# Kernel tuning notes

Measured on AMD Instinct MI355X. Metric: run time of the kernel, lower is better.

## Reference

```python
import jax, jax.numpy as jnp
import numpy as np

N, K, D = 65536, 4096, 64


def setup_inputs() -> dict:
    key = jax.random.key(0)
    kx, ke = jax.random.split(key)
    x = jax.random.normal(kx, (N, D), dtype=jnp.float32)
    embed = jax.random.normal(ke, (1, K, D), dtype=jnp.float32)
    return {"x": x, "embed": embed}


def reference(x, embed):
    # Faithful to EuclideanCodebook.forward quantization path:
    #   dist = cdist(flatten, embed, p=2)**2 ; argmin ; one_hot @ embed
    xf = x.astype(jnp.float32)            # [N, D]
    e = embed[0]                          # [K, D]
    # squared euclidean distance via expansion (== cdist(...).pow(2))
    x_sq = jnp.sum(xf * xf, axis=-1, keepdims=True)        # [N, 1]
    e_sq = jnp.sum(e * e, axis=-1)                          # [K]
    dist = jnp.maximum(x_sq + e_sq[None, :] - 2.0 * (xf @ e.T), 0.0)  # [N, K]
    embed_ind = jnp.argmin(dist, axis=-1)                   # [N]
    # one_hot @ embed is exactly a row gather of the codebook
    quantize = e[embed_ind]                                 # [N, D]
    return quantize, embed_ind[None, :]                     # embed_ind kept as [1, N] like torch
```

## Files before the change

### kernel.cpp

```cpp
#include <hip/hip_runtime.h>
#include <math.h>

#define N_ROWS 65536
#define K_CODES 4096
#define NTILES_TOTAL (K_CODES / 32)
#define K_CHUNKS 2
#define NTILES (NTILES_TOTAL / K_CHUNKS)
#define DIM 64
#define NBUF 4
#define ACC_MARGIN 0.005f

typedef __attribute__((ext_vector_type(8))) short bf16x8;
typedef __attribute__((ext_vector_type(4))) float f32x4;

__device__ inline unsigned short f2bf_rne(float f) {
    unsigned u = __float_as_uint(f);
    return (unsigned short)((u + 0x7FFFu + ((u >> 16) & 1u)) >> 16);
}
__device__ inline float bf2f(unsigned short s) {
    return __uint_as_float(((unsigned)s) << 16);
}

__global__ __launch_bounds__(256) void pack_e(const float* __restrict__ embed,
                                              short* __restrict__ e_pk,
                                              float* __restrict__ esq,
                                              float* __restrict__ esqn,
                                              int* __restrict__ count) {
    __shared__ float lds_f[2048];
    const int tile = blockIdx.x;
    const int t = threadIdx.x;
    if (tile == 0 && t == 0) *count = 0;
    const float4* src = (const float4*)(embed + (size_t)tile * 2048);
    ((float4*)lds_f)[t] = src[t];
    ((float4*)lds_f)[t + 256] = src[t + 256];
    __syncthreads();
    const int l = t & 63;
    const int kh = (t >> 6) & 1;
    const int ch = (t >> 7) & 1;
    const int base = (ch * 16 + (l & 15)) * 64 + kh * 32 + ((l >> 4) & 3) * 8;
    bf16x8 vh, vl;
#pragma unroll
    for (int j = 0; j < 8; ++j) {
        float v = lds_f[base + j];
        unsigned short h = f2bf_rne(v);
        vh[j] = (short)h;
        vl[j] = (short)f2bf_rne(v - bf2f(h));
    }
    *(bf16x8*)(e_pk + (size_t)tile * 4096 + t * 8) = vh;
    *(bf16x8*)(e_pk + (size_t)tile * 4096 + 2048 + t * 8) = vl;
    if (t < 32) {
        float s = 0.f;
#pragma unroll
        for (int d = 0; d < 64; ++d) { float v = lds_f[t * 64 + d]; s = fmaf(v, v, s); }
        esq[tile * 32 + t] = s;
        esqn[tile * 32 + t] = -0.5f * s;
    }
}

__global__ __launch_bounds__(256, 4) void vq_main(const float* __restrict__ x,
                                                  const short* __restrict__ e_pk,
                                                  const float* __restrict__ esqn,
                                                  float* __restrict__ b1s,
                                                  float* __restrict__ b2s,
                                                  int* __restrict__ i1s) {
    __shared__ __align__(16) char lds[NBUF][8192];
    __shared__ __align__(16) float lds_q[NBUF][64];
    const int tid = threadIdx.x;
    const int wid = tid >> 6;
    const int l = tid & 63;
    const int c16 = l & 15;
    const int rgrp = (l >> 4) & 3;
    const int kc = blockIdx.x & (K_CHUNKS - 1);
    const int rg = blockIdx.x >> 1;
    const int rowbase = rg * 128 + wid * 32;
    const int tile0 = kc * NTILES;

    bf16x8 ah[2][2], al[2][2];
#pragma unroll
    for (int rh = 0; rh < 2; ++rh) {
        const float* xr = x + (size_t)(rowbase + rh * 16 + c16) * DIM;
#pragma unroll
        for (int kh = 0; kh < 2; ++kh) {
            const float* p = xr + kh * 32 + rgrp * 8;
#pragma unroll
            for (int j = 0; j < 8; ++j) {
                float v = p[j];
                unsigned short h = f2bf_rne(v);
                ah[rh][kh][j] = (short)h;
                al[rh][kh][j] = (short)f2bf_rne(v - bf2f(h));
            }
        }
    }

    float b1[8], b2[8];
    int i1[8];
#pragma unroll
    for (int i = 0; i < 8; ++i) { b1[i] = -3.0e38f; b2[i] = -3.0e38f; i1[i] = 0; }

    auto stage = [&](int t, int b) {
        const char* gsrc = (const char*)e_pk + (size_t)(tile0 + t) * 8192 + tid * 16;
        __builtin_amdgcn_global_load_lds(
            (const __attribute__((address_space(1))) void*)gsrc,
            (__attribute__((address_space(3))) void*)(&lds[b][wid * 1024]), 16, 0, 0);
        __builtin_amdgcn_global_load_lds(
            (const __attribute__((address_space(1))) void*)(gsrc + 4096),
            (__attribute__((address_space(3))) void*)(&lds[b][4096 + wid * 1024]), 16, 0, 0);
        const float* qsrc = esqn + (size_t)(tile0 + t) * 32 + l;
        __builtin_amdgcn_global_load_lds(
            (const __attribute__((address_space(1))) void*)qsrc,
            (__attribute__((address_space(3))) void*)(&lds_q[b][0]), 4, 0, 0);
    };

    stage(0, 0);
    stage(1, 1);

    for (int t = 0; t < NTILES; ++t) {
        const int cur = t & (NBUF - 1);
        if (t + 2 < NTILES) stage(t + 2, (t + 2) & (NBUF - 1));
        asm volatile("s_waitcnt vmcnt(6)" ::: "memory");
        __builtin_amdgcn_sched_barrier(0);
        __builtin_amdgcn_s_barrier();
        __builtin_amdgcn_sched_barrier(0);

        const float eq0 = lds_q[cur][c16];
        const float eq1 = lds_q[cur][16 + c16];
        const int ci0 = (tile0 + t) * 32 + c16;
        const int ci1 = ci0 + 16;

        f32x4 a00 = {eq0, eq0, eq0, eq0};
        f32x4 a01 = {eq1, eq1, eq1, eq1};
        f32x4 a10 = {eq0, eq0, eq0, eq0};
        f32x4 a11 = {eq1, eq1, eq1, eq1};

        __builtin_amdgcn_s_setprio(1);
#pragma unroll
        for (int kh = 0; kh < 2; ++kh) {
            const int fo0 = ((0 * 2 + kh) * 64 + l) * 16;
            const int fo1 = ((1 * 2 + kh) * 64 + l) * 16;
            const bf16x8 bh0 = *(const bf16x8*)(&lds[cur][fo0]);
            const bf16x8 bh1 = *(const bf16x8*)(&lds[cur][fo1]);
            const bf16x8 bl0 = *(const bf16x8*)(&lds[cur][4096 + fo0]);
            const bf16x8 bl1 = *(const bf16x8*)(&lds[cur][4096 + fo1]);
            a00 = __builtin_amdgcn_mfma_f32_16x16x32_bf16(ah[0][kh], bh0, a00, 0, 0, 0);
            a01 = __builtin_amdgcn_mfma_f32_16x16x32_bf16(ah[0][kh], bh1, a01, 0, 0, 0);
            a10 = __builtin_amdgcn_mfma_f32_16x16x32_bf16(ah[1][kh], bh0, a10, 0, 0, 0);
            a11 = __builtin_amdgcn_mfma_f32_16x16x32_bf16(ah[1][kh], bh1, a11, 0, 0, 0);
            a00 = __builtin_amdgcn_mfma_f32_16x16x32_bf16(ah[0][kh], bl0, a00, 0, 0, 0);
            a01 = __builtin_amdgcn_mfma_f32_16x16x32_bf16(ah[0][kh], bl1, a01, 0, 0, 0);
            a10 = __builtin_amdgcn_mfma_f32_16x16x32_bf16(ah[1][kh], bl0, a10, 0, 0, 0);
            a11 = __builtin_amdgcn_mfma_f32_16x16x32_bf16(ah[1][kh], bl1, a11, 0, 0, 0);
            a00 = __builtin_amdgcn_mfma_f32_16x16x32_bf16(al[0][kh], bh0, a00, 0, 0, 0);
            a01 = __builtin_amdgcn_mfma_f32_16x16x32_bf16(al[0][kh], bh1, a01, 0, 0, 0);
            a10 = __builtin_amdgcn_mfma_f32_16x16x32_bf16(al[1][kh], bh0, a10, 0, 0, 0);
            a11 = __builtin_amdgcn_mfma_f32_16x16x32_bf16(al[1][kh], bh1, a11, 0, 0, 0);
        }
        __builtin_amdgcn_s_setprio(0);

#define TRACK2(V0, V1, E)                                            \
        {                                                            \
            float v0 = (V0), v1 = (V1);                              \
            bool g0 = v0 > b1[E];                                    \
            b2[E] = __builtin_amdgcn_fmed3f(v0, b1[E], b2[E]);       \
            b1[E] = fmaxf(v0, b1[E]);                                \
            i1[E] = g0 ? ci0 : i1[E];                                \
            bool g1 = v1 > b1[E];                                    \
            b2[E] = __builtin_amdgcn_fmed3f(v1, b1[E], b2[E]);       \
            b1[E] = fmaxf(v1, b1[E]);                                \
            i1[E] = g1 ? ci1 : i1[E];                                \
        }
#pragma unroll
        for (int j = 0; j < 4; ++j) {
            TRACK2(a00[j], a01[j], j)
            TRACK2(a10[j], a11[j], 4 + j)
        }
#undef TRACK2
    }

#pragma unroll
    for (int e = 0; e < 8; ++e) {
#pragma unroll
        for (int m = 1; m <= 8; m <<= 1) {
            float ob1 = __shfl_xor(b1[e], m);
            float ob2 = __shfl_xor(b2[e], m);
            int oi = __shfl_xor(i1[e], m);
            float nb2 = fmaxf(fminf(b1[e], ob1), fmaxf(b2[e], ob2));
            bool take = ob1 > b1[e];
            b1[e] = take ? ob1 : b1[e];
            i1[e] = take ? oi : i1[e];
            b2[e] = nb2;
        }
        if (c16 == 0) {
            int row = rowbase + (e >> 2) * 16 + rgrp * 4 + (e & 3);
            b1s[(size_t)kc * N_ROWS + row] = b1[e];
            b2s[(size_t)kc * N_ROWS + row] = b2[e];
            i1s[(size_t)kc * N_ROWS + row] = i1[e];
        }
    }
}

__global__ __launch_bounds__(256) void vq_merge_gather(const float* __restrict__ embed,
                                                       const float* __restrict__ b1s,
                                                       const float* __restrict__ b2s,
                                                       const int* __restrict__ i1s,
                                                       float* __restrict__ out_q,
                                                       float* __restrict__ out_ind,
                                                       int* __restrict__ list,
                                                       int* __restrict__ count) {
    int t = blockIdx.x * 256 + threadIdx.x;
    int r = t >> 3, q = t & 7;
    float ab1 = b1s[r], bb1 = b1s[N_ROWS + r];
    float ab2 = b2s[r], bb2 = b2s[N_ROWS + r];
    int ai = i1s[r], bi = i1s[N_ROWS + r];
    bool take = bb1 > ab1;
    int idx = take ? bi : ai;
    float m1 = fmaxf(ab1, bb1);
    float m2 = fmaxf(fminf(ab1, bb1), fmaxf(ab2, bb2));
    const float4* src = (const float4*)(embed + (size_t)idx * DIM + q * 8);
    float4* dst = (float4*)(out_q + (size_t)r * DIM + q * 8);
    dst[0] = src[0];
    dst[1] = src[1];
    if (q == 0) {
        out_ind[r] = (float)idx;
        if (m1 - m2 < ACC_MARGIN) {
            int p = atomicAdd(count, 1);
            list[p] = r;
        }
    }
}

__global__ __launch_bounds__(256) void vq_rescore(const float* __restrict__ x,
                                                  const float* __restrict__ embed,
                                                  const float* __restrict__ esq,
                                                  const int* __restrict__ list,
                                                  const int* __restrict__ count,
                                                  float* __restrict__ out_q,
                                                  float* __restrict__ out_ind) {
    __shared__ float xs[64];
    __shared__ float sk[256];
    __shared__ int si[256];
    const int tid = threadIdx.x;
    const int n = *count;
    for (int f = blockIdx.x; f < n; f += gridDim.x) {
        const int row = list[f];
        if (tid < 16) ((float4*)xs)[tid] = ((const float4*)(x + (size_t)row * DIM))[tid];
        __syncthreads();
        float best = 3.0e38f;
        int bi = 0;
        for (int i = 0; i < 16; ++i) {
            int c = tid + (i << 8);
            const float* e = embed + (size_t)c * DIM;
            float d0 = 0, d1 = 0, d2 = 0, d3 = 0;
#pragma unroll
            for (int d = 0; d < 64; d += 4) {
                d0 = fmaf(xs[d + 0], e[d + 0], d0);
                d1 = fmaf(xs[d + 1], e[d + 1], d1);
                d2 = fmaf(xs[d + 2], e[d + 2], d2);
                d3 = fmaf(xs[d + 3], e[d + 3], d3);
            }
            float key = fmaf(-2.f, (d0 + d1) + (d2 + d3), esq[c]);
            if (key < best) { best = key; bi = c; }
        }
        sk[tid] = best; si[tid] = bi;
        __syncthreads();
        for (int s = 128; s > 0; s >>= 1) {
            if (tid < s) {
                float ok = sk[tid + s]; int oi = si[tid + s];
                if (ok < sk[tid] || (ok == sk[tid] && oi < si[tid])) { sk[tid] = ok; si[tid] = oi; }
            }
            __syncthreads();
        }
        if (tid == 0) out_ind[row] = (float)si[0];
        if (tid < 16) {
            const float4* src = (const float4*)(embed + (size_t)si[0] * DIM);
            ((float4*)(out_q + (size_t)row * DIM))[tid] = src[tid];
        }
        __syncthreads();
    }
}

extern "C" void kernel_launch(void* const* d_in, const int* in_sizes, int n_in,
                              void* d_out, int out_size, void* d_ws, size_t ws_size,
                              hipStream_t stream) {
    const float* x = (const float*)d_in[0];
    const float* embed = (const float*)d_in[1];
    float* out = (float*)d_out;
    float* out_ind = out + (size_t)N_ROWS * DIM;

    char* ws = (char*)d_ws;
    short* e_pk = (short*)ws;
    size_t off = 1 << 20;
    float* esq = (float*)(ws + off);  off += 17 << 10;
    float* esqn = (float*)(ws + off); off += 17 << 10;
    float* b1s = (float*)(ws + off);  off += (size_t)K_CHUNKS * N_ROWS * 4;
    float* b2s = (float*)(ws + off);  off += (size_t)K_CHUNKS * N_ROWS * 4;
    int* i1s = (int*)(ws + off);      off += (size_t)K_CHUNKS * N_ROWS * 4;
    int* list = (int*)(ws + off);     off += (size_t)N_ROWS * 4;
    int* count = (int*)(ws + off);

    pack_e<<<NTILES_TOTAL, 256, 0, stream>>>(embed, e_pk, esq, esqn, count);
    vq_main<<<(N_ROWS / 128) * K_CHUNKS, 256, 0, stream>>>(x, e_pk, esqn, b1s, b2s, i1s);
    vq_merge_gather<<<N_ROWS * 8 / 256, 256, 0, stream>>>(embed, b1s, b2s, i1s,
                                                          out, out_ind, list, count);
    vq_rescore<<<512, 256, 0, stream>>>(x, embed, esq, list, count, out, out_ind);
}
```

Baseline: 146.9 us.

## Switch codebook LDS staging to double buffer with full wait and hoisted fragment loads

```diff
diff --git a/kernel.cpp b/kernel.cpp
--- a/kernel.cpp
+++ b/kernel.cpp
@@ -7,7 +7,7 @@
 #define K_CHUNKS 2
 #define NTILES (NTILES_TOTAL / K_CHUNKS)
 #define DIM 64
-#define NBUF 4
+#define NBUF 2
 #define ACC_MARGIN 0.005f
 
 typedef __attribute__((ext_vector_type(8))) short bf16x8;
@@ -112,21 +112,30 @@
     };
 
     stage(0, 0);
-    stage(1, 1);
 
     for (int t = 0; t < NTILES; ++t) {
-        const int cur = t & (NBUF - 1);
-        if (t + 2 < NTILES) stage(t + 2, (t + 2) & (NBUF - 1));
-        asm volatile("s_waitcnt vmcnt(6)" ::: "memory");
+        const int cur = t & 1;
+        asm volatile("s_waitcnt vmcnt(0) lgkmcnt(0)" ::: "memory");
         __builtin_amdgcn_sched_barrier(0);
         __builtin_amdgcn_s_barrier();
         __builtin_amdgcn_sched_barrier(0);
+        if (t + 1 < NTILES) stage(t + 1, cur ^ 1);
 
         const float eq0 = lds_q[cur][c16];
         const float eq1 = lds_q[cur][16 + c16];
         const int ci0 = (tile0 + t) * 32 + c16;
         const int ci1 = ci0 + 16;
 
+        bf16x8 bh[2][2], bl[2][2];
+#pragma unroll
+        for (int ch = 0; ch < 2; ++ch)
+#pragma unroll
+            for (int kh = 0; kh < 2; ++kh) {
+                const int fo = ((ch * 2 + kh) * 64 + l) * 16;
+                bh[ch][kh] = *(const bf16x8*)(&lds[cur][fo]);
+                bl[ch][kh] = *(const bf16x8*)(&lds[cur][4096 + fo]);
+            }
+
         f32x4 a00 = {eq0, eq0, eq0, eq0};
         f32x4 a01 = {eq1, eq1, eq1, eq1};
         f32x4 a10 = {eq0, eq0, eq0, eq0};
@@ -135,24 +144,18 @@
         __builtin_amdgcn_s_setprio(1);
 #pragma unroll
         for (int kh = 0; kh < 2; ++kh) {
-            const int fo0 = ((0 * 2 + kh) * 64 + l) * 16;
-            const int fo1 = ((1 * 2 + kh) * 64 + l) * 16;
-            const bf16x8 bh0 = *(const bf16x8*)(&lds[cur][fo0]);
-            const bf16x8 bh1 = *(const bf16x8*)(&lds[cur][fo1]);
-            const bf16x8 bl0 = *(const bf16x8*)(&lds[cur][4096 + fo0]);
-            const bf16x8 bl1 = *(const bf16x8*)(&lds[cur][4096 + fo1]);
-            a00 = __builtin_amdgcn_mfma_f32_16x16x32_bf16(ah[0][kh], bh0, a00, 0, 0, 0);
-            a01 = __builtin_amdgcn_mfma_f32_16x16x32_bf16(ah[0][kh], bh1, a01, 0, 0, 0);
-            a10 = __builtin_amdgcn_mfma_f32_16x16x32_bf16(ah[1][kh], bh0, a10, 0, 0, 0);
-            a11 = __builtin_amdgcn_mfma_f32_16x16x32_bf16(ah[1][kh], bh1, a11, 0, 0, 0);
-            a00 = __builtin_amdgcn_mfma_f32_16x16x32_bf16(ah[0][kh], bl0, a00, 0, 0, 0);
-            a01 = __builtin_amdgcn_mfma_f32_16x16x32_bf16(ah[0][kh], bl1, a01, 0, 0, 0);
-            a10 = __builtin_amdgcn_mfma_f32_16x16x32_bf16(ah[1][kh], bl0, a10, 0, 0, 0);
-            a11 = __builtin_amdgcn_mfma_f32_16x16x32_bf16(ah[1][kh], bl1, a11, 0, 0, 0);
-            a00 = __builtin_amdgcn_mfma_f32_16x16x32_bf16(al[0][kh], bh0, a00, 0, 0, 0);
-            a01 = __builtin_amdgcn_mfma_f32_16x16x32_bf16(al[0][kh], bh1, a01, 0, 0, 0);
-            a10 = __builtin_amdgcn_mfma_f32_16x16x32_bf16(al[1][kh], bh0, a10, 0, 0, 0);
-            a11 = __builtin_amdgcn_mfma_f32_16x16x32_bf16(al[1][kh], bh1, a11, 0, 0, 0);
+            a00 = __builtin_amdgcn_mfma_f32_16x16x32_bf16(ah[0][kh], bh[0][kh], a00, 0, 0, 0);
+            a01 = __builtin_amdgcn_mfma_f32_16x16x32_bf16(ah[0][kh], bh[1][kh], a01, 0, 0, 0);
+            a10 = __builtin_amdgcn_mfma_f32_16x16x32_bf16(ah[1][kh], bh[0][kh], a10, 0, 0, 0);
+            a11 = __builtin_amdgcn_mfma_f32_16x16x32_bf16(ah[1][kh], bh[1][kh], a11, 0, 0, 0);
+            a00 = __builtin_amdgcn_mfma_f32_16x16x32_bf16(ah[0][kh], bl[0][kh], a00, 0, 0, 0);
+            a01 = __builtin_amdgcn_mfma_f32_16x16x32_bf16(ah[0][kh], bl[1][kh], a01, 0, 0, 0);
+            a10 = __builtin_amdgcn_mfma_f32_16x16x32_bf16(ah[1][kh], bl[0][kh], a10, 0, 0, 0);
+            a11 = __builtin_amdgcn_mfma_f32_16x16x32_bf16(ah[1][kh], bl[1][kh], a11, 0, 0, 0);
+            a00 = __builtin_amdgcn_mfma_f32_16x16x32_bf16(al[0][kh], bh[0][kh], a00, 0, 0, 0);
+            a01 = __builtin_amdgcn_mfma_f32_16x16x32_bf16(al[0][kh], bh[1][kh], a01, 0, 0, 0);
+            a10 = __builtin_amdgcn_mfma_f32_16x16x32_bf16(al[1][kh], bh[0][kh], a10, 0, 0, 0);
+            a11 = __builtin_amdgcn_mfma_f32_16x16x32_bf16(al[1][kh], bh[1][kh], a11, 0, 0, 0);
         }
         __builtin_amdgcn_s_setprio(0);
 
```

After: 146.5 us. Within noise of the previous version (-0.2%).

## Double per-wave row tile and load codebook tiles directly to registers

Applied to the files above, without the earlier changes.

```diff
diff --git a/kernel.cpp b/kernel.cpp
--- a/kernel.cpp
+++ b/kernel.cpp
@@ -7,7 +7,6 @@
 #define K_CHUNKS 2
 #define NTILES (NTILES_TOTAL / K_CHUNKS)
 #define DIM 64
-#define NBUF 4
 #define ACC_MARGIN 0.005f
 
 typedef __attribute__((ext_vector_type(8))) short bf16x8;
@@ -57,14 +56,12 @@
     }
 }
 
-__global__ __launch_bounds__(256, 4) void vq_main(const float* __restrict__ x,
+__global__ __launch_bounds__(256, 2) void vq_main(const float* __restrict__ x,
                                                   const short* __restrict__ e_pk,
                                                   const float* __restrict__ esqn,
                                                   float* __restrict__ b1s,
                                                   float* __restrict__ b2s,
                                                   int* __restrict__ i1s) {
-    __shared__ __align__(16) char lds[NBUF][8192];
-    __shared__ __align__(16) float lds_q[NBUF][64];
     const int tid = threadIdx.x;
     const int wid = tid >> 6;
     const int l = tid & 63;
@@ -72,12 +69,12 @@
     const int rgrp = (l >> 4) & 3;
     const int kc = blockIdx.x & (K_CHUNKS - 1);
     const int rg = blockIdx.x >> 1;
-    const int rowbase = rg * 128 + wid * 32;
+    const int rowbase = rg * 256 + wid * 64;
     const int tile0 = kc * NTILES;
 
-    bf16x8 ah[2][2], al[2][2];
-#pragma unroll
-    for (int rh = 0; rh < 2; ++rh) {
+    bf16x8 ah[4][2], al[4][2];
+#pragma unroll
+    for (int rh = 0; rh < 4; ++rh) {
         const float* xr = x + (size_t)(rowbase + rh * 16 + c16) * DIM;
 #pragma unroll
         for (int kh = 0; kh < 2; ++kh) {
@@ -92,92 +89,89 @@
         }
     }
 
-    float b1[8], b2[8];
-    int i1[8];
-#pragma unroll
-    for (int i = 0; i < 8; ++i) { b1[i] = -3.0e38f; b2[i] = -3.0e38f; i1[i] = 0; }
-
-    auto stage = [&](int t, int b) {
-        const char* gsrc = (const char*)e_pk + (size_t)(tile0 + t) * 8192 + tid * 16;
-        __builtin_amdgcn_global_load_lds(
-            (const __attribute__((address_space(1))) void*)gsrc,
-            (__attribute__((address_space(3))) void*)(&lds[b][wid * 1024]), 16, 0, 0);
-        __builtin_amdgcn_global_load_lds(
-            (const __attribute__((address_space(1))) void*)(gsrc + 4096),
-            (__attribute__((address_space(3))) void*)(&lds[b][4096 + wid * 1024]), 16, 0, 0);
-        const float* qsrc = esqn + (size_t)(tile0 + t) * 32 + l;
-        __builtin_amdgcn_global_load_lds(
-            (const __attribute__((address_space(1))) void*)qsrc,
-            (__attribute__((address_space(3))) void*)(&lds_q[b][0]), 4, 0, 0);
-    };
-
-    stage(0, 0);
-    stage(1, 1);
-
-    for (int t = 0; t < NTILES; ++t) {
-        const int cur = t & (NBUF - 1);
-        if (t + 2 < NTILES) stage(t + 2, (t + 2) & (NBUF - 1));
-        asm volatile("s_waitcnt vmcnt(6)" ::: "memory");
-        __builtin_amdgcn_sched_barrier(0);
-        __builtin_amdgcn_s_barrier();
-        __builtin_amdgcn_sched_barrier(0);
-
-        const float eq0 = lds_q[cur][c16];
-        const float eq1 = lds_q[cur][16 + c16];
-        const int ci0 = (tile0 + t) * 32 + c16;
-        const int ci1 = ci0 + 16;
-
-        f32x4 a00 = {eq0, eq0, eq0, eq0};
-        f32x4 a01 = {eq1, eq1, eq1, eq1};
-        f32x4 a10 = {eq0, eq0, eq0, eq0};
-        f32x4 a11 = {eq1, eq1, eq1, eq1};
-
-        __builtin_amdgcn_s_setprio(1);
-#pragma unroll
-        for (int kh = 0; kh < 2; ++kh) {
-            const int fo0 = ((0 * 2 + kh) * 64 + l) * 16;
-            const int fo1 = ((1 * 2 + kh) * 64 + l) * 16;
-            const bf16x8 bh0 = *(const bf16x8*)(&lds[cur][fo0]);
-            const bf16x8 bh1 = *(const bf16x8*)(&lds[cur][fo1]);
-            const bf16x8 bl0 = *(const bf16x8*)(&lds[cur][4096 + fo0]);
-            const bf16x8 bl1 = *(const bf16x8*)(&lds[cur][4096 + fo1]);
-            a00 = __builtin_amdgcn_mfma_f32_16x16x32_bf16(ah[0][kh], bh0, a00, 0, 0, 0);
-            a01 = __builtin_amdgcn_mfma_f32_16x16x32_bf16(ah[0][kh], bh1, a01, 0, 0, 0);
-            a10 = __builtin_amdgcn_mfma_f32_16x16x32_bf16(ah[1][kh], bh0, a10, 0, 0, 0);
-            a11 = __builtin_amdgcn_mfma_f32_16x16x32_bf16(ah[1][kh], bh1, a11, 0, 0, 0);
-            a00 = __builtin_amdgcn_mfma_f32_16x16x32_bf16(ah[0][kh], bl0, a00, 0, 0, 0);
-            a01 = __builtin_amdgcn_mfma_f32_16x16x32_bf16(ah[0][kh], bl1, a01, 0, 0, 0);
-            a10 = __builtin_amdgcn_mfma_f32_16x16x32_bf16(ah[1][kh], bl0, a10, 0, 0, 0);
-            a11 = __builtin_amdgcn_mfma_f32_16x16x32_bf16(ah[1][kh], bl1, a11, 0, 0, 0);
-            a00 = __builtin_amdgcn_mfma_f32_16x16x32_bf16(al[0][kh], bh0, a00, 0, 0, 0);
-            a01 = __builtin_amdgcn_mfma_f32_16x16x32_bf16(al[0][kh], bh1, a01, 0, 0, 0);
-            a10 = __builtin_amdgcn_mfma_f32_16x16x32_bf16(al[1][kh], bh0, a10, 0, 0, 0);
-            a11 = __builtin_amdgcn_mfma_f32_16x16x32_bf16(al[1][kh], bh1, a11, 0, 0, 0);
-        }
-        __builtin_amdgcn_s_setprio(0);
-
-#define TRACK2(V0, V1, E)                                            \
+    float b1[16], b2[16];
+    int i1[16];
+#pragma unroll
+    for (int i = 0; i < 16; ++i) { b1[i] = -3.0e38f; b2[i] = -3.0e38f; i1[i] = 0; }
+
+    const bf16x8* ep = (const bf16x8*)e_pk;
+
+#define LOADB(TT, BH, BL, EQ0, EQ1)                                  \
+    {                                                                \
+        const bf16x8* bp = ep + (size_t)(TT) * 512;                  \
+        _Pragma("unroll")                                            \
+        for (int ch = 0; ch < 2; ++ch)                               \
+            _Pragma("unroll")                                        \
+            for (int kh = 0; kh < 2; ++kh) {                         \
+                BH[ch][kh] = bp[(ch * 2 + kh) * 64 + l];             \
+                BL[ch][kh] = bp[256 + (ch * 2 + kh) * 64 + l];       \
+            }                                                        \
+        EQ0 = esqn[(TT) * 32 + c16];                                 \
+        EQ1 = esqn[(TT) * 32 + 16 + c16];                            \
+    }
+
+#define TRACK2(V0, V1, E, CI0, CI1)                                  \
         {                                                            \
             float v0 = (V0), v1 = (V1);                              \
             bool g0 = v0 > b1[E];                                    \
             b2[E] = __builtin_amdgcn_fmed3f(v0, b1[E], b2[E]);       \
             b1[E] = fmaxf(v0, b1[E]);                                \
-            i1[E] = g0 ? ci0 : i1[E];                                \
+            i1[E] = g0 ? (CI0) : i1[E];                              \
             bool g1 = v1 > b1[E];                                    \
             b2[E] = __builtin_amdgcn_fmed3f(v1, b1[E], b2[E]);       \
             b1[E] = fmaxf(v1, b1[E]);                                \
-            i1[E] = g1 ? ci1 : i1[E];                                \
-        }
-#pragma unroll
-        for (int j = 0; j < 4; ++j) {
-            TRACK2(a00[j], a01[j], j)
-            TRACK2(a10[j], a11[j], 4 + j)
-        }
+            i1[E] = g1 ? (CI1) : i1[E];                              \
+        }
+
+#define COMPUTE(TT, BH, BL, EQ0, EQ1)                                \
+    {                                                                \
+        const int ci0 = (TT) * 32 + c16;                             \
+        const int ci1 = ci0 + 16;                                    \
+        f32x4 acc[4][2];                                             \
+        _Pragma("unroll")                                            \
+        for (int rh = 0; rh < 4; ++rh) {                             \
+            acc[rh][0] = (f32x4){EQ0, EQ0, EQ0, EQ0};                \
+            acc[rh][1] = (f32x4){EQ1, EQ1, EQ1, EQ1};                \
+        }                                                            \
+        __builtin_amdgcn_s_setprio(1);                               \
+        _Pragma("unroll")                                            \
+        for (int kh = 0; kh < 2; ++kh)                               \
+            _Pragma("unroll")                                        \
+            for (int rh = 0; rh < 4; ++rh) {                         \
+                acc[rh][0] = __builtin_amdgcn_mfma_f32_16x16x32_bf16(ah[rh][kh], BH[0][kh], acc[rh][0], 0, 0, 0); \
+                acc[rh][1] = __builtin_amdgcn_mfma_f32_16x16x32_bf16(ah[rh][kh], BH[1][kh], acc[rh][1], 0, 0, 0); \
+                acc[rh][0] = __builtin_amdgcn_mfma_f32_16x16x32_bf16(ah[rh][kh], BL[0][kh], acc[rh][0], 0, 0, 0); \
+                acc[rh][1] = __builtin_amdgcn_mfma_f32_16x16x32_bf16(ah[rh][kh], BL[1][kh], acc[rh][1], 0, 0, 0); \
+                acc[rh][0] = __builtin_amdgcn_mfma_f32_16x16x32_bf16(al[rh][kh], BH[0][kh], acc[rh][0], 0, 0, 0); \
+                acc[rh][1] = __builtin_amdgcn_mfma_f32_16x16x32_bf16(al[rh][kh], BH[1][kh], acc[rh][1], 0, 0, 0); \
+            }                                                        \
+        __builtin_amdgcn_s_setprio(0);                               \
+        _Pragma("unroll")                                            \
+        for (int rh = 0; rh < 4; ++rh)                               \
+            _Pragma("unroll")                                        \
+            for (int j = 0; j < 4; ++j)                              \
+                TRACK2(acc[rh][0][j], acc[rh][1][j], rh * 4 + j, ci0, ci1) \
+    }
+
+    bf16x8 bhA[2][2], blA[2][2], bhB[2][2], blB[2][2];
+    float eqA0, eqA1, eqB0, eqB1;
+
+    LOADB(tile0, bhA, blA, eqA0, eqA1);
+#pragma unroll 1
+    for (int t = 0; t < NTILES; t += 2) {
+        const int gt1 = tile0 + t + 1;
+        const int gt2 = tile0 + min(t + 2, NTILES - 1);
+        LOADB(gt1, bhB, blB, eqB0, eqB1);
+        COMPUTE(tile0 + t, bhA, blA, eqA0, eqA1);
+        LOADB(gt2, bhA, blA, eqA0, eqA1);
+        COMPUTE(gt1, bhB, blB, eqB0, eqB1);
+    }
+#undef LOADB
+#undef COMPUTE
 #undef TRACK2
-    }
-
-#pragma unroll
-    for (int e = 0; e < 8; ++e) {
+
+#pragma unroll
+    for (int e = 0; e < 16; ++e) {
 #pragma unroll
         for (int m = 1; m <= 8; m <<= 1) {
             float ob1 = __shfl_xor(b1[e], m);
@@ -298,7 +292,7 @@
     int* count = (int*)(ws + off);
 
     pack_e<<<NTILES_TOTAL, 256, 0, stream>>>(embed, e_pk, esq, esqn, count);
-    vq_main<<<(N_ROWS / 128) * K_CHUNKS, 256, 0, stream>>>(x, e_pk, esqn, b1s, b2s, i1s);
+    vq_main<<<(N_ROWS / 256) * K_CHUNKS, 256, 0, stream>>>(x, e_pk, esqn, b1s, b2s, i1s);
     vq_merge_gather<<<N_ROWS * 8 / 256, 256, 0, stream>>>(embed, b1s, b2s, i1s,
                                                           out, out_ind, list, count);
     vq_rescore<<<512, 256, 0, stream>>>(x, embed, esq, list, count, out, out_ind);
```

Result: faster. 139.6 us (-4.9%).
